# Kernel optimization log

Hardware: AMD Instinct MI355X
Metric: run time of the kernel (lower is better)

The kernel has to match this reference:

```python
import jax, jax.numpy as jnp
import numpy as np

B, N_SMI, N_ATOM, N_PROT, D = 8, 100, 45, 1000, 64


def setup_inputs() -> dict:
    key = jax.random.key(0)
    ks = jax.random.split(key, 8)
    return {
        "smi_tf": jax.random.normal(ks[0], (B, N_SMI, D), dtype=jnp.float32),
        "pro_tf": jax.random.normal(ks[1], (B, N_PROT, D), dtype=jnp.float32),
        "drug_gat": jax.random.normal(ks[2], (B, N_ATOM, D), dtype=jnp.float32),
        "w_att": jax.random.normal(ks[3], (D, D), dtype=jnp.float32) * 0.05,
        "b_att": jnp.zeros((D,), dtype=jnp.float32),
        "w1": jax.random.normal(ks[4], (2 * D, 1024), dtype=jnp.float32) * 0.05,
        "b1": jnp.zeros((1024,), dtype=jnp.float32),
        "w2": jax.random.normal(ks[5], (1024, 1024), dtype=jnp.float32) * 0.05,
        "b2": jnp.zeros((1024,), dtype=jnp.float32),
        "w3": jax.random.normal(ks[6], (1024, 512), dtype=jnp.float32) * 0.05,
        "b3": jnp.zeros((512,), dtype=jnp.float32),
        "w4": jax.random.normal(ks[7], (512, 2), dtype=jnp.float32) * 0.05,
        "b4": jnp.zeros((2,), dtype=jnp.float32),
    }


def reference(smi_tf, pro_tf, drug_gat, w_att, b_att, w1, b1, w2, b2, w3, b3, w4, b4):
    # shared attention projection on both streams
    smi_att = smi_tf @ w_att + b_att            # (B, N_smi, D)
    pro_att = pro_tf @ w_att + b_att            # (B, N_prot, D)
    smi_attss = jnp.concatenate([smi_att, drug_gat], axis=1)  # (B, Nd, D)

    # pairwise broadcast add + relu + shared linear (the big intermediate)
    pair = jax.nn.relu(smi_attss[:, :, None, :] + pro_att[:, None, :, :])  # (B, Nd, Np, D)
    atten = pair @ w_att + b_att                                           # (B, Nd, Np, D)

    # dual mean-pool gates
    smi_atts = jax.nn.sigmoid(atten.mean(axis=2))   # (B, Nd, D)
    pro_atts = jax.nn.sigmoid(atten.mean(axis=1))   # (B, Np, D)

    smi_tfs = 0.5 * smi_attss + smi_attss * smi_atts
    pro_tfs = 0.5 * pro_tf + pro_tf * pro_atts

    smi = smi_tfs.mean(axis=1)   # (B, D)
    pro = pro_tfs.mean(axis=1)   # (B, D)
    x = jnp.concatenate([smi, pro], axis=-1)  # (B, 2D)

    x = jax.nn.relu(x @ w1 + b1)
    x = jax.nn.relu(x @ w2 + b2)
    x = jax.nn.relu(x @ w3 + b3)
    return x @ w4 + b4  # (B, 2)
```

## Files before the change

kernel.cpp:

```cpp
#include <hip/hip_runtime.h>
#include <math.h>

#define B 8
#define NSMI 100
#define NATOM 45
#define ND 145
#define NP 1000
#define D 64
#define NROW 1145

#define PROJ_RPB 16
#define PROJ_BPB 72
#define ROW_BPB 37
#define COL_BPB 250
#define PAIR_ROW_BLKS (B * ROW_BPB)
#define PAIR_BLKS (PAIR_ROW_BLKS + B * COL_BPB)

__device__ __forceinline__ float4 f4z() { float4 z; z.x = z.y = z.z = z.w = 0.f; return z; }
__device__ __forceinline__ void f4acc(float4& a, const float4& v) {
    a.x += v.x; a.y += v.y; a.z += v.z; a.w += v.w;
}
__device__ __forceinline__ void acc_relu(float4& acc, const float4& a, const float4& p) {
    acc.x += fmaxf(0.f, a.x + p.x);
    acc.y += fmaxf(0.f, a.y + p.y);
    acc.z += fmaxf(0.f, a.z + p.z);
    acc.w += fmaxf(0.f, a.w + p.w);
}
__device__ __forceinline__ void wave_red_g(float4& v) {
    v.x += __shfl_xor(v.x, 16, 64); v.x += __shfl_xor(v.x, 32, 64);
    v.y += __shfl_xor(v.y, 16, 64); v.y += __shfl_xor(v.y, 32, 64);
    v.z += __shfl_xor(v.z, 16, 64); v.z += __shfl_xor(v.z, 32, 64);
    v.w += __shfl_xor(v.w, 16, 64); v.w += __shfl_xor(v.w, 32, 64);
}

__global__ __launch_bounds__(256) void k_proj2(
    const float* __restrict__ smi_tf, const float* __restrict__ pro_tf,
    const float* __restrict__ drug_gat, const float* __restrict__ w_att,
    const float* __restrict__ b_att,
    float* __restrict__ smi_attss, float* __restrict__ pro_att)
{
    int blk = blockIdx.x, t = threadIdx.x;
    int b = blk / PROJ_BPB;
    int r0 = (blk - b * PROJ_BPB) * PROJ_RPB;

    __shared__ float4 wl[64 * 17];
    __shared__ float4 rl4[16 * 17];

    #pragma unroll
    for (int i2 = 0; i2 < 4; ++i2) {
        int f = t + 256 * i2;
        float4 v = ((const float4*)w_att)[f];
        wl[(f >> 4) * 17 + (f & 15)] = v;
    }
    int rl = t >> 4, p = t & 15;
    int r = r0 + rl;
    {
        float4 v = f4z();
        if (r < NROW) {
            const float* src;
            if (r < NSMI)      src = smi_tf   + (size_t)(b * NSMI + r) * D;
            else if (r < ND)   src = drug_gat + (size_t)(b * NATOM + (r - NSMI)) * D;
            else               src = pro_tf   + (size_t)(b * NP + (r - ND)) * D;
            v = ((const float4*)src)[p];
        }
        rl4[rl * 17 + p] = v;
    }
    __syncthreads();
    if (r >= NROW) return;
    float4 out;
    if (r >= NSMI && r < ND) {
        out = rl4[rl * 17 + p];
    } else {
        float4 acc = ((const float4*)b_att)[p];
        const float* rowf = (const float*)rl4;
        #pragma unroll
        for (int k = 0; k < 64; ++k) {
            float val = rowf[rl * 68 + k];
            float4 w = wl[k * 17 + p];
            acc.x = fmaf(val, w.x, acc.x);
            acc.y = fmaf(val, w.y, acc.y);
            acc.z = fmaf(val, w.z, acc.z);
            acc.w = fmaf(val, w.w, acc.w);
        }
        out = acc;
    }
    if (r < ND) ((float4*)smi_attss)[(size_t)(b * ND + r) * 16 + p] = out;
    else        ((float4*)pro_att)[(size_t)(b * NP + (r - ND)) * 16 + p] = out;
}

__global__ __launch_bounds__(512) void k_pair(
    const float4* __restrict__ smi4, const float4* __restrict__ pro4,
    const float* __restrict__ smi_attss, const float* __restrict__ pro_tf,
    const float* __restrict__ w_att, const float* __restrict__ b_att,
    float* __restrict__ smi_tfs, float* __restrict__ pro_tfs)
{
    __shared__ float4 red[8][4][16];
    __shared__ float vl[4][64];
    int blk = blockIdx.x, t = threadIdx.x;
    int w = t >> 6, lane = t & 63, l = lane & 15, g = lane >> 4;
    int u = w * 4 + g;
    float4 acc0 = f4z(), acc1 = f4z(), acc2 = f4z(), acc3 = f4z();
    int b, base;
    bool isRow = (blk < PAIR_ROW_BLKS);

    if (isRow) {
        b = blk / ROW_BPB;
        base = (blk - b * ROW_BPB) * 4;
        float4 a0 = (base + 0 < ND) ? smi4[(size_t)(b * ND + base + 0) * 16 + l] : f4z();
        float4 a1 = (base + 1 < ND) ? smi4[(size_t)(b * ND + base + 1) * 16 + l] : f4z();
        float4 a2 = (base + 2 < ND) ? smi4[(size_t)(b * ND + base + 2) * 16 + l] : f4z();
        float4 a3 = (base + 3 < ND) ? smi4[(size_t)(b * ND + base + 3) * 16 + l] : f4z();
        const float4* pp = pro4 + (size_t)b * NP * 16 + u * 16 + l;
        #pragma unroll 4
        for (int it = 0; it < 31; ++it) {
            float4 pv = pp[it * 512];
            acc_relu(acc0, a0, pv); acc_relu(acc1, a1, pv);
            acc_relu(acc2, a2, pv); acc_relu(acc3, a3, pv);
        }
        if (u < 8) {
            float4 pv = pp[31 * 512];
            acc_relu(acc0, a0, pv); acc_relu(acc1, a1, pv);
            acc_relu(acc2, a2, pv); acc_relu(acc3, a3, pv);
        }
    } else {
        int cb = blk - PAIR_ROW_BLKS;
        b = cb / COL_BPB;
        base = (cb - b * COL_BPB) * 4;
        float4 p0 = pro4[(size_t)(b * NP + base + 0) * 16 + l];
        float4 p1 = pro4[(size_t)(b * NP + base + 1) * 16 + l];
        float4 p2 = pro4[(size_t)(b * NP + base + 2) * 16 + l];
        float4 p3 = pro4[(size_t)(b * NP + base + 3) * 16 + l];
        const float4* ap = smi4 + (size_t)b * ND * 16 + u * 16 + l;
        #pragma unroll
        for (int it = 0; it < 4; ++it) {
            float4 av = ap[it * 512];
            acc_relu(acc0, av, p0); acc_relu(acc1, av, p1);
            acc_relu(acc2, av, p2); acc_relu(acc3, av, p3);
        }
        if (u < 17) {
            float4 av = ap[4 * 512];
            acc_relu(acc0, av, p0); acc_relu(acc1, av, p1);
            acc_relu(acc2, av, p2); acc_relu(acc3, av, p3);
        }
    }

    wave_red_g(acc0); wave_red_g(acc1); wave_red_g(acc2); wave_red_g(acc3);
    if (lane < 16) {
        red[w][0][l] = acc0; red[w][1][l] = acc1;
        red[w][2][l] = acc2; red[w][3][l] = acc3;
    }
    __syncthreads();
    float invn = isRow ? (1.0f / NP) : (1.0f / ND);
    if (t < 64) {
        int ii = t >> 4, l2 = t & 15;
        float4 s = f4z();
        #pragma unroll
        for (int w2 = 0; w2 < 8; ++w2) f4acc(s, red[w2][ii][l2]);
        vl[ii][l2 * 4 + 0] = s.x * invn;
        vl[ii][l2 * 4 + 1] = s.y * invn;
        vl[ii][l2 * 4 + 2] = s.z * invn;
        vl[ii][l2 * 4 + 3] = s.w * invn;
    }
    __syncthreads();
    if (t < 256) {
        int ii = t >> 6, d = t & 63;
        int r = base + ii;
        bool ok = isRow ? (r < ND) : true;
        if (ok) {
            float m = b_att[d];
            #pragma unroll
            for (int k = 0; k < 64; ++k) m = fmaf(vl[ii][k], w_att[k * 64 + d], m);
            float gs = 1.f / (1.f + expf(-m));
            if (isRow) {
                size_t idx = (size_t)(b * ND + r) * 64 + d;
                smi_tfs[idx] = smi_attss[idx] * (0.5f + gs);
            } else {
                size_t idx = (size_t)(b * NP + r) * 64 + d;
                pro_tfs[idx] = pro_tf[idx] * (0.5f + gs);
            }
        }
    }
}

__global__ __launch_bounds__(512) void k_pool(
    const float4* __restrict__ smi_tfs4, const float4* __restrict__ pro_tfs4,
    float* __restrict__ x)
{
    __shared__ float4 ldsb[1024];
    int blk = blockIdx.x, t = threadIdx.x;
    int b = blk >> 4, s = blk & 15;
    float4 sa = f4z(), pa = f4z();
    if (t < ND) f4acc(sa, smi_tfs4[(size_t)(b * ND + t) * 16 + s]);
    for (int j = t; j < NP; j += 512) f4acc(pa, pro_tfs4[(size_t)(b * NP + j) * 16 + s]);
    ldsb[t] = sa; ldsb[512 + t] = pa;
    __syncthreads();
    for (int st = 256; st > 0; st >>= 1) {
        if (t < st) { f4acc(ldsb[t], ldsb[t + st]); f4acc(ldsb[512 + t], ldsb[512 + t + st]); }
        __syncthreads();
    }
    if (t == 0) {
        float4 S = ldsb[0], P = ldsb[512];
        x[b * 128 + s * 4 + 0] = S.x * (1.0f / ND);
        x[b * 128 + s * 4 + 1] = S.y * (1.0f / ND);
        x[b * 128 + s * 4 + 2] = S.z * (1.0f / ND);
        x[b * 128 + s * 4 + 3] = S.w * (1.0f / ND);
        x[b * 128 + 64 + s * 4 + 0] = P.x * (1.0f / NP);
        x[b * 128 + 64 + s * 4 + 1] = P.y * (1.0f / NP);
        x[b * 128 + 64 + s * 4 + 2] = P.z * (1.0f / NP);
        x[b * 128 + 64 + s * 4 + 3] = P.w * (1.0f / NP);
    }
}

__global__ __launch_bounds__(256) void k_l1(
    const float4* __restrict__ x4, const float4* __restrict__ w1_4,
    const float4* __restrict__ b1_4, float4* __restrict__ h1_4)
{
    __shared__ float lds_x[1024];
    __shared__ float4 red[2048];
    int oc = blockIdx.x, t = threadIdx.x;
    ((float4*)lds_x)[t] = x4[t];
    __syncthreads();
    int ol = t & 15, g = t >> 4;
    int o4 = oc * 16 + ol;
    float4 acc[8];
    #pragma unroll
    for (int b = 0; b < 8; ++b) acc[b] = f4z();
    #pragma unroll
    for (int kk = 0; kk < 8; ++kk) {
        int k = g * 8 + kk;
        float4 wv = w1_4[(size_t)k * 256 + o4];
        #pragma unroll
        for (int b = 0; b < 8; ++b) {
            float xv = lds_x[b * 128 + k];
            acc[b].x = fmaf(xv, wv.x, acc[b].x);
            acc[b].y = fmaf(xv, wv.y, acc[b].y);
            acc[b].z = fmaf(xv, wv.z, acc[b].z);
            acc[b].w = fmaf(xv, wv.w, acc[b].w);
        }
    }
    #pragma unroll
    for (int b = 0; b < 8; ++b) red[g * 128 + ol * 8 + b] = acc[b];
    __syncthreads();
    int u = t & 127, gg = t >> 7;
    float4 s = f4z();
    #pragma unroll
    for (int j = 0; j < 8; ++j) f4acc(s, red[(gg * 8 + j) * 128 + u]);
    red[gg * 8 * 128 + u] = s;
    __syncthreads();
    if (t < 128) {
        float4 v = red[t];
        f4acc(v, red[1024 + t]);
        int olr = t >> 3, b = t & 7;
        float4 bb = b1_4[oc * 16 + olr];
        v.x = fmaxf(v.x + bb.x, 0.f); v.y = fmaxf(v.y + bb.y, 0.f);
        v.z = fmaxf(v.z + bb.z, 0.f); v.w = fmaxf(v.w + bb.w, 0.f);
        h1_4[b * 256 + oc * 16 + olr] = v;
    }
}

__global__ __launch_bounds__(512) void k_l2(
    const float4* __restrict__ h1_4, const float4* __restrict__ w2_4,
    const float4* __restrict__ b2_4, float4* __restrict__ h2_4)
{
    __shared__ float4 buf[4096];
    float* lds_h = (float*)buf;
    int oc = blockIdx.x, t = threadIdx.x;
    #pragma unroll
    for (int j = 0; j < 4; ++j) buf[t + 512 * j] = h1_4[t + 512 * j];
    __syncthreads();
    int ol = t & 3, g = t >> 2;
    int o4 = oc * 4 + ol;
    float4 acc[8];
    #pragma unroll
    for (int b = 0; b < 8; ++b) acc[b] = f4z();
    #pragma unroll
    for (int kk = 0; kk < 8; ++kk) {
        int k = g * 8 + kk;
        float4 wv = w2_4[(size_t)k * 256 + o4];
        #pragma unroll
        for (int b = 0; b < 8; ++b) {
            float hv = lds_h[b * 1024 + k];
            acc[b].x = fmaf(hv, wv.x, acc[b].x);
            acc[b].y = fmaf(hv, wv.y, acc[b].y);
            acc[b].z = fmaf(hv, wv.z, acc[b].z);
            acc[b].w = fmaf(hv, wv.w, acc[b].w);
        }
    }
    __syncthreads();
    #pragma unroll
    for (int b = 0; b < 8; ++b) buf[g * 32 + ol * 8 + b] = acc[b];
    __syncthreads();
    int u = t & 31, gg = t >> 5;
    float4 s = f4z();
    #pragma unroll
    for (int j = 0; j < 8; ++j) f4acc(s, buf[(gg * 8 + j) * 32 + u]);
    buf[gg * 256 + u] = s;
    __syncthreads();
    if (t < 32) {
        float4 v = f4z();
        #pragma unroll
        for (int gg2 = 0; gg2 < 16; ++gg2) f4acc(v, buf[gg2 * 256 + t]);
        int olr = t >> 3, b = t & 7;
        float4 bb = b2_4[oc * 4 + olr];
        v.x = fmaxf(v.x + bb.x, 0.f); v.y = fmaxf(v.y + bb.y, 0.f);
        v.z = fmaxf(v.z + bb.z, 0.f); v.w = fmaxf(v.w + bb.w, 0.f);
        h2_4[b * 256 + oc * 4 + olr] = v;
    }
}

__global__ __launch_bounds__(512) void k_l3(
    const float4* __restrict__ h2_4, const float4* __restrict__ w3_4,
    const float4* __restrict__ b3_4, float4* __restrict__ h3_4)
{
    __shared__ float4 buf[4096];
    float* lds_h = (float*)buf;
    int oc = blockIdx.x, t = threadIdx.x;
    #pragma unroll
    for (int j = 0; j < 4; ++j) buf[t + 512 * j] = h2_4[t + 512 * j];
    __syncthreads();
    int ol = t & 3, g = t >> 2;
    int o4 = oc * 4 + ol;
    float4 acc[8];
    #pragma unroll
    for (int b = 0; b < 8; ++b) acc[b] = f4z();
    #pragma unroll
    for (int kk = 0; kk < 8; ++kk) {
        int k = g * 8 + kk;
        float4 wv = w3_4[(size_t)k * 128 + o4];
        #pragma unroll
        for (int b = 0; b < 8; ++b) {
            float hv = lds_h[b * 1024 + k];
            acc[b].x = fmaf(hv, wv.x, acc[b].x);
            acc[b].y = fmaf(hv, wv.y, acc[b].y);
            acc[b].z = fmaf(hv, wv.z, acc[b].z);
            acc[b].w = fmaf(hv, wv.w, acc[b].w);
        }
    }
    __syncthreads();
    #pragma unroll
    for (int b = 0; b < 8; ++b) buf[g * 32 + ol * 8 + b] = acc[b];
    __syncthreads();
    int u = t & 31, gg = t >> 5;
    float4 s = f4z();
    #pragma unroll
    for (int j = 0; j < 8; ++j) f4acc(s, buf[(gg * 8 + j) * 32 + u]);
    buf[gg * 256 + u] = s;
    __syncthreads();
    if (t < 32) {
        float4 v = f4z();
        #pragma unroll
        for (int gg2 = 0; gg2 < 16; ++gg2) f4acc(v, buf[gg2 * 256 + t]);
        int olr = t >> 3, b = t & 7;
        float4 bb = b3_4[oc * 4 + olr];
        v.x = fmaxf(v.x + bb.x, 0.f); v.y = fmaxf(v.y + bb.y, 0.f);
        v.z = fmaxf(v.z + bb.z, 0.f); v.w = fmaxf(v.w + bb.w, 0.f);
        h3_4[b * 128 + oc * 4 + olr] = v;
    }
}

__global__ __launch_bounds__(512) void k_l4(
    const float* __restrict__ h3, const float* __restrict__ w4p,
    const float* __restrict__ b4p, float* __restrict__ out)
{
    __shared__ float h3s[4096];
    __shared__ float w4s[1024];
    __shared__ float red[8][8][2];
    int t = threadIdx.x;
    ((float4*)h3s)[t] = ((const float4*)h3)[t];
    ((float4*)h3s)[t + 512] = ((const float4*)h3)[t + 512];
    if (t < 256) ((float4*)w4s)[t] = ((const float4*)w4p)[t];
    __syncthreads();
    int w = t >> 6, lane = t & 63;
    #pragma unroll
    for (int b = 0; b < 8; ++b) {
        float hv = h3s[b * 512 + t];
        float v0 = hv * w4s[t * 2];
        float v1 = hv * w4s[t * 2 + 1];
        #pragma unroll
        for (int off = 32; off > 0; off >>= 1) {
            v0 += __shfl_xor(v0, off, 64);
            v1 += __shfl_xor(v1, off, 64);
        }
        if (lane == 0) { red[w][b][0] = v0; red[w][b][1] = v1; }
    }
    __syncthreads();
    if (t < 16) {
        int b = t >> 1, o = t & 1;
        float s = b4p[o];
        #pragma unroll
        for (int w2 = 0; w2 < 8; ++w2) s += red[w2][b][o];
        out[b * 2 + o] = s;
    }
}

extern "C" void kernel_launch(void* const* d_in, const int* in_sizes, int n_in,
                              void* d_out, int out_size, void* d_ws, size_t ws_size,
                              hipStream_t stream)
{
    const float* smi_tf   = (const float*)d_in[0];
    const float* pro_tf   = (const float*)d_in[1];
    const float* drug_gat = (const float*)d_in[2];
    const float* w_att    = (const float*)d_in[3];
    const float* b_att    = (const float*)d_in[4];
    const float* w1 = (const float*)d_in[5];
    const float* b1 = (const float*)d_in[6];
    const float* w2 = (const float*)d_in[7];
    const float* b2 = (const float*)d_in[8];
    const float* w3 = (const float*)d_in[9];
    const float* b3 = (const float*)d_in[10];
    const float* w4 = (const float*)d_in[11];
    const float* b4 = (const float*)d_in[12];
    float* out = (float*)d_out;

    float* ws = (float*)d_ws;
    float* smi_attss = ws;
    float* pro_att   = smi_attss + 74240;
    float* smi_tfs   = pro_att + 512000;
    float* pro_tfs   = smi_tfs + 74240;
    float* x   = pro_tfs + 512000;
    float* h1  = x + 1024;
    float* h2  = h1 + 8192;
    float* h3  = h2 + 8192;

    k_proj2<<<B * PROJ_BPB, 256, 0, stream>>>(smi_tf, pro_tf, drug_gat, w_att, b_att,
                                              smi_attss, pro_att);
    k_pair <<<PAIR_BLKS, 512, 0, stream>>>((const float4*)smi_attss, (const float4*)pro_att,
                                           smi_attss, pro_tf, w_att, b_att, smi_tfs, pro_tfs);
    k_pool <<<128, 512, 0, stream>>>((const float4*)smi_tfs, (const float4*)pro_tfs, x);
    k_l1   <<<16, 256, 0, stream>>>((const float4*)x, (const float4*)w1,
                                    (const float4*)b1, (float4*)h1);
    k_l2   <<<64, 512, 0, stream>>>((const float4*)h1, (const float4*)w2,
                                    (const float4*)b2, (float4*)h2);
    k_l3   <<<32, 512, 0, stream>>>((const float4*)h2, (const float4*)w3,
                                    (const float4*)b3, (float4*)h3);
    k_l4   <<<1, 512, 0, stream>>>(h3, w4, b4, out);
}
```

Before: 129.8 us.

## Fuse pooling into pair kernel via atomics and merge MLP layers

The gated outputs are no longer written to global memory and re-read by a separate pooling kernel. The pair kernel now reduces its four rows in shared memory and atomically adds column sums into a small buffer, which the projection kernel zeroes. Layer 1 is recomputed redundantly in every block of the fused layer 1+2 kernel, and layers 3 and 4 are fused with atomic accumulation into the output. Seven launches become four, at the cost of atomic contention and redundant layer-1 work, and the float sums are no longer deterministic.

```diff
diff --git a/kernel.cpp b/kernel.cpp
--- a/kernel.cpp
+++ b/kernel.cpp
@@ -37,9 +37,14 @@
     const float* __restrict__ smi_tf, const float* __restrict__ pro_tf,
     const float* __restrict__ drug_gat, const float* __restrict__ w_att,
     const float* __restrict__ b_att,
-    float* __restrict__ smi_attss, float* __restrict__ pro_att)
+    float* __restrict__ smi_attss, float* __restrict__ pro_att,
+    float* __restrict__ x_sums, float* __restrict__ out)
 {
     int blk = blockIdx.x, t = threadIdx.x;
+    if (blk == 0) {
+        ((float4*)x_sums)[t] = f4z();
+        if (t < 16) out[t] = 0.f;
+    }
     int b = blk / PROJ_BPB;
     int r0 = (blk - b * PROJ_BPB) * PROJ_RPB;
 
@@ -67,9 +72,9 @@
     }
     __syncthreads();
     if (r >= NROW) return;
-    float4 out;
+    float4 out4;
     if (r >= NSMI && r < ND) {
-        out = rl4[rl * 17 + p];
+        out4 = rl4[rl * 17 + p];
     } else {
         float4 acc = ((const float4*)b_att)[p];
         const float* rowf = (const float*)rl4;
@@ -82,20 +87,21 @@
             acc.z = fmaf(val, w.z, acc.z);
             acc.w = fmaf(val, w.w, acc.w);
         }
-        out = acc;
-    }
-    if (r < ND) ((float4*)smi_attss)[(size_t)(b * ND + r) * 16 + p] = out;
-    else        ((float4*)pro_att)[(size_t)(b * NP + (r - ND)) * 16 + p] = out;
+        out4 = acc;
+    }
+    if (r < ND) ((float4*)smi_attss)[(size_t)(b * ND + r) * 16 + p] = out4;
+    else        ((float4*)pro_att)[(size_t)(b * NP + (r - ND)) * 16 + p] = out4;
 }
 
 __global__ __launch_bounds__(512) void k_pair(
     const float4* __restrict__ smi4, const float4* __restrict__ pro4,
     const float* __restrict__ smi_attss, const float* __restrict__ pro_tf,
     const float* __restrict__ w_att, const float* __restrict__ b_att,
-    float* __restrict__ smi_tfs, float* __restrict__ pro_tfs)
+    float* __restrict__ x_sums)
 {
     __shared__ float4 red[8][4][16];
     __shared__ float vl[4][64];
+    __shared__ float gv[4][64];
     int blk = blockIdx.x, t = threadIdx.x;
     int w = t >> 6, lane = t & 63, l = lane & 15, g = lane >> 4;
     int u = w * 4 + g;
@@ -166,107 +172,122 @@
         int ii = t >> 6, d = t & 63;
         int r = base + ii;
         bool ok = isRow ? (r < ND) : true;
+        float v = 0.f;
         if (ok) {
             float m = b_att[d];
             #pragma unroll
             for (int k = 0; k < 64; ++k) m = fmaf(vl[ii][k], w_att[k * 64 + d], m);
             float gs = 1.f / (1.f + expf(-m));
-            if (isRow) {
-                size_t idx = (size_t)(b * ND + r) * 64 + d;
-                smi_tfs[idx] = smi_attss[idx] * (0.5f + gs);
-            } else {
-                size_t idx = (size_t)(b * NP + r) * 64 + d;
-                pro_tfs[idx] = pro_tf[idx] * (0.5f + gs);
-            }
-        }
-    }
-}
-
-__global__ __launch_bounds__(512) void k_pool(
-    const float4* __restrict__ smi_tfs4, const float4* __restrict__ pro_tfs4,
-    float* __restrict__ x)
-{
-    __shared__ float4 ldsb[1024];
-    int blk = blockIdx.x, t = threadIdx.x;
-    int b = blk >> 4, s = blk & 15;
-    float4 sa = f4z(), pa = f4z();
-    if (t < ND) f4acc(sa, smi_tfs4[(size_t)(b * ND + t) * 16 + s]);
-    for (int j = t; j < NP; j += 512) f4acc(pa, pro_tfs4[(size_t)(b * NP + j) * 16 + s]);
-    ldsb[t] = sa; ldsb[512 + t] = pa;
-    __syncthreads();
-    for (int st = 256; st > 0; st >>= 1) {
-        if (t < st) { f4acc(ldsb[t], ldsb[t + st]); f4acc(ldsb[512 + t], ldsb[512 + t + st]); }
-        __syncthreads();
-    }
-    if (t == 0) {
-        float4 S = ldsb[0], P = ldsb[512];
-        x[b * 128 + s * 4 + 0] = S.x * (1.0f / ND);
-        x[b * 128 + s * 4 + 1] = S.y * (1.0f / ND);
-        x[b * 128 + s * 4 + 2] = S.z * (1.0f / ND);
-        x[b * 128 + s * 4 + 3] = S.w * (1.0f / ND);
-        x[b * 128 + 64 + s * 4 + 0] = P.x * (1.0f / NP);
-        x[b * 128 + 64 + s * 4 + 1] = P.y * (1.0f / NP);
-        x[b * 128 + 64 + s * 4 + 2] = P.z * (1.0f / NP);
-        x[b * 128 + 64 + s * 4 + 3] = P.w * (1.0f / NP);
-    }
-}
-
-__global__ __launch_bounds__(256) void k_l1(
-    const float4* __restrict__ x4, const float4* __restrict__ w1_4,
-    const float4* __restrict__ b1_4, float4* __restrict__ h1_4)
-{
-    __shared__ float lds_x[1024];
-    __shared__ float4 red[2048];
+            size_t idx = isRow ? ((size_t)(b * ND + r) * 64 + d)
+                               : ((size_t)(b * NP + r) * 64 + d);
+            v = (isRow ? smi_attss[idx] : pro_tf[idx]) * (0.5f + gs);
+        }
+        gv[ii][d] = v;
+    }
+    __syncthreads();
+    if (t < 64) {
+        float s = gv[0][t] + gv[1][t] + gv[2][t] + gv[3][t];
+        atomicAdd(&x_sums[b * 128 + (isRow ? 0 : 64) + t], s);
+    }
+}
+
+__global__ __launch_bounds__(512) void k_l12(
+    const float* __restrict__ x_sums, const float4* __restrict__ w1_4,
+    const float* __restrict__ b1, const float4* __restrict__ w2_4,
+    const float* __restrict__ b2, float4* __restrict__ h2_4)
+{
+    __shared__ float4 buf[4096];
+    float* xs  = (float*)buf;
+    float* h1f = (float*)buf + 1024;
+    float4* h1f4 = buf + 256;
     int oc = blockIdx.x, t = threadIdx.x;
-    ((float4*)lds_x)[t] = x4[t];
-    __syncthreads();
-    int ol = t & 15, g = t >> 4;
-    int o4 = oc * 16 + ol;
+    xs[t]       = x_sums[t]       * (((t & 127) < 64) ? (1.0f / ND) : (1.0f / NP));
+    xs[t + 512] = x_sums[t + 512] * (((t & 127) < 64) ? (1.0f / ND) : (1.0f / NP));
+    __syncthreads();
+    {
+        int o4 = t & 255, bh = t >> 8;
+        const float* x0 = xs + (bh * 4 + 0) * 128;
+        const float* x1 = xs + (bh * 4 + 1) * 128;
+        const float* x2 = xs + (bh * 4 + 2) * 128;
+        const float* x3 = xs + (bh * 4 + 3) * 128;
+        float4 a0 = f4z(), a1 = f4z(), a2 = f4z(), a3 = f4z();
+        #pragma unroll 8
+        for (int k = 0; k < 128; ++k) {
+            float4 wv = w1_4[(size_t)k * 256 + o4];
+            a0.x = fmaf(x0[k], wv.x, a0.x); a0.y = fmaf(x0[k], wv.y, a0.y);
+            a0.z = fmaf(x0[k], wv.z, a0.z); a0.w = fmaf(x0[k], wv.w, a0.w);
+            a1.x = fmaf(x1[k], wv.x, a1.x); a1.y = fmaf(x1[k], wv.y, a1.y);
+            a1.z = fmaf(x1[k], wv.z, a1.z); a1.w = fmaf(x1[k], wv.w, a1.w);
+            a2.x = fmaf(x2[k], wv.x, a2.x); a2.y = fmaf(x2[k], wv.y, a2.y);
+            a2.z = fmaf(x2[k], wv.z, a2.z); a2.w = fmaf(x2[k], wv.w, a2.w);
+            a3.x = fmaf(x3[k], wv.x, a3.x); a3.y = fmaf(x3[k], wv.y, a3.y);
+            a3.z = fmaf(x3[k], wv.z, a3.z); a3.w = fmaf(x3[k], wv.w, a3.w);
+        }
+        float4 bb = ((const float4*)b1)[o4];
+        a0.x = fmaxf(a0.x + bb.x, 0.f); a0.y = fmaxf(a0.y + bb.y, 0.f);
+        a0.z = fmaxf(a0.z + bb.z, 0.f); a0.w = fmaxf(a0.w + bb.w, 0.f);
+        a1.x = fmaxf(a1.x + bb.x, 0.f); a1.y = fmaxf(a1.y + bb.y, 0.f);
+        a1.z = fmaxf(a1.z + bb.z, 0.f); a1.w = fmaxf(a1.w + bb.w, 0.f);
+        a2.x = fmaxf(a2.x + bb.x, 0.f); a2.y = fmaxf(a2.y + bb.y, 0.f);
+        a2.z = fmaxf(a2.z + bb.z, 0.f); a2.w = fmaxf(a2.w + bb.w, 0.f);
+        a3.x = fmaxf(a3.x + bb.x, 0.f); a3.y = fmaxf(a3.y + bb.y, 0.f);
+        a3.z = fmaxf(a3.z + bb.z, 0.f); a3.w = fmaxf(a3.w + bb.w, 0.f);
+        h1f4[(size_t)(bh * 4 + 0) * 256 + o4] = a0;
+        h1f4[(size_t)(bh * 4 + 1) * 256 + o4] = a1;
+        h1f4[(size_t)(bh * 4 + 2) * 256 + o4] = a2;
+        h1f4[(size_t)(bh * 4 + 3) * 256 + o4] = a3;
+    }
+    __syncthreads();
+    int ol = t & 3, g = t >> 2;
+    int o4g = oc * 4 + ol;
     float4 acc[8];
     #pragma unroll
     for (int b = 0; b < 8; ++b) acc[b] = f4z();
     #pragma unroll
     for (int kk = 0; kk < 8; ++kk) {
         int k = g * 8 + kk;
-        float4 wv = w1_4[(size_t)k * 256 + o4];
+        float4 wv = w2_4[(size_t)k * 256 + o4g];
         #pragma unroll
         for (int b = 0; b < 8; ++b) {
-            float xv = lds_x[b * 128 + k];
-            acc[b].x = fmaf(xv, wv.x, acc[b].x);
-            acc[b].y = fmaf(xv, wv.y, acc[b].y);
-            acc[b].z = fmaf(xv, wv.z, acc[b].z);
-            acc[b].w = fmaf(xv, wv.w, acc[b].w);
-        }
-    }
-    #pragma unroll
-    for (int b = 0; b < 8; ++b) red[g * 128 + ol * 8 + b] = acc[b];
-    __syncthreads();
-    int u = t & 127, gg = t >> 7;
+            float hv = h1f[b * 1024 + k];
+            acc[b].x = fmaf(hv, wv.x, acc[b].x);
+            acc[b].y = fmaf(hv, wv.y, acc[b].y);
+            acc[b].z = fmaf(hv, wv.z, acc[b].z);
+            acc[b].w = fmaf(hv, wv.w, acc[b].w);
+        }
+    }
+    __syncthreads();
+    #pragma unroll
+    for (int b = 0; b < 8; ++b) buf[g * 32 + ol * 8 + b] = acc[b];
+    __syncthreads();
+    int u = t & 31, gg = t >> 5;
     float4 s = f4z();
     #pragma unroll
-    for (int j = 0; j < 8; ++j) f4acc(s, red[(gg * 8 + j) * 128 + u]);
-    red[gg * 8 * 128 + u] = s;
-    __syncthreads();
-    if (t < 128) {
-        float4 v = red[t];
-        f4acc(v, red[1024 + t]);
+    for (int j = 0; j < 8; ++j) f4acc(s, buf[(gg * 8 + j) * 32 + u]);
+    buf[gg * 256 + u] = s;
+    __syncthreads();
+    if (t < 32) {
+        float4 v = f4z();
+        #pragma unroll
+        for (int gg2 = 0; gg2 < 16; ++gg2) f4acc(v, buf[gg2 * 256 + t]);
         int olr = t >> 3, b = t & 7;
-        float4 bb = b1_4[oc * 16 + olr];
+        float4 bb = ((const float4*)b2)[oc * 4 + olr];
         v.x = fmaxf(v.x + bb.x, 0.f); v.y = fmaxf(v.y + bb.y, 0.f);
         v.z = fmaxf(v.z + bb.z, 0.f); v.w = fmaxf(v.w + bb.w, 0.f);
-        h1_4[b * 256 + oc * 16 + olr] = v;
-    }
-}
-
-__global__ __launch_bounds__(512) void k_l2(
-    const float4* __restrict__ h1_4, const float4* __restrict__ w2_4,
-    const float4* __restrict__ b2_4, float4* __restrict__ h2_4)
+        h2_4[b * 256 + oc * 4 + olr] = v;
+    }
+}
+
+__global__ __launch_bounds__(512) void k_l34(
+    const float4* __restrict__ h2_4, const float4* __restrict__ w3_4,
+    const float* __restrict__ b3, const float* __restrict__ w4p,
+    const float* __restrict__ b4p, float* __restrict__ out)
 {
     __shared__ float4 buf[4096];
     float* lds_h = (float*)buf;
     int oc = blockIdx.x, t = threadIdx.x;
     #pragma unroll
-    for (int j = 0; j < 4; ++j) buf[t + 512 * j] = h1_4[t + 512 * j];
+    for (int j = 0; j < 4; ++j) buf[t + 512 * j] = h2_4[t + 512 * j];
     __syncthreads();
     int ol = t & 3, g = t >> 2;
     int o4 = oc * 4 + ol;
@@ -276,7 +297,7 @@
     #pragma unroll
     for (int kk = 0; kk < 8; ++kk) {
         int k = g * 8 + kk;
-        float4 wv = w2_4[(size_t)k * 256 + o4];
+        float4 wv = w3_4[(size_t)k * 128 + o4];
         #pragma unroll
         for (int b = 0; b < 8; ++b) {
             float hv = lds_h[b * 1024 + k];
@@ -301,95 +322,21 @@
         #pragma unroll
         for (int gg2 = 0; gg2 < 16; ++gg2) f4acc(v, buf[gg2 * 256 + t]);
         int olr = t >> 3, b = t & 7;
-        float4 bb = b2_4[oc * 4 + olr];
+        float4 bb = ((const float4*)b3)[oc * 4 + olr];
         v.x = fmaxf(v.x + bb.x, 0.f); v.y = fmaxf(v.y + bb.y, 0.f);
         v.z = fmaxf(v.z + bb.z, 0.f); v.w = fmaxf(v.w + bb.w, 0.f);
-        h2_4[b * 256 + oc * 4 + olr] = v;
-    }
-}
-
-__global__ __launch_bounds__(512) void k_l3(
-    const float4* __restrict__ h2_4, const float4* __restrict__ w3_4,
-    const float4* __restrict__ b3_4, float4* __restrict__ h3_4)
-{
-    __shared__ float4 buf[4096];
-    float* lds_h = (float*)buf;
-    int oc = blockIdx.x, t = threadIdx.x;
-    #pragma unroll
-    for (int j = 0; j < 4; ++j) buf[t + 512 * j] = h2_4[t + 512 * j];
-    __syncthreads();
-    int ol = t & 3, g = t >> 2;
-    int o4 = oc * 4 + ol;
-    float4 acc[8];
-    #pragma unroll
-    for (int b = 0; b < 8; ++b) acc[b] = f4z();
-    #pragma unroll
-    for (int kk = 0; kk < 8; ++kk) {
-        int k = g * 8 + kk;
-        float4 wv = w3_4[(size_t)k * 128 + o4];
-        #pragma unroll
-        for (int b = 0; b < 8; ++b) {
-            float hv = lds_h[b * 1024 + k];
-            acc[b].x = fmaf(hv, wv.x, acc[b].x);
-            acc[b].y = fmaf(hv, wv.y, acc[b].y);
-            acc[b].z = fmaf(hv, wv.z, acc[b].z);
-            acc[b].w = fmaf(hv, wv.w, acc[b].w);
-        }
-    }
-    __syncthreads();
-    #pragma unroll
-    for (int b = 0; b < 8; ++b) buf[g * 32 + ol * 8 + b] = acc[b];
-    __syncthreads();
-    int u = t & 31, gg = t >> 5;
-    float4 s = f4z();
-    #pragma unroll
-    for (int j = 0; j < 8; ++j) f4acc(s, buf[(gg * 8 + j) * 32 + u]);
-    buf[gg * 256 + u] = s;
-    __syncthreads();
-    if (t < 32) {
-        float4 v = f4z();
-        #pragma unroll
-        for (int gg2 = 0; gg2 < 16; ++gg2) f4acc(v, buf[gg2 * 256 + t]);
-        int olr = t >> 3, b = t & 7;
-        float4 bb = b3_4[oc * 4 + olr];
-        v.x = fmaxf(v.x + bb.x, 0.f); v.y = fmaxf(v.y + bb.y, 0.f);
-        v.z = fmaxf(v.z + bb.z, 0.f); v.w = fmaxf(v.w + bb.w, 0.f);
-        h3_4[b * 128 + oc * 4 + olr] = v;
-    }
-}
-
-__global__ __launch_bounds__(512) void k_l4(
-    const float* __restrict__ h3, const float* __restrict__ w4p,
-    const float* __restrict__ b4p, float* __restrict__ out)
-{
-    __shared__ float h3s[4096];
-    __shared__ float w4s[1024];
-    __shared__ float red[8][8][2];
-    int t = threadIdx.x;
-    ((float4*)h3s)[t] = ((const float4*)h3)[t];
-    ((float4*)h3s)[t + 512] = ((const float4*)h3)[t + 512];
-    if (t < 256) ((float4*)w4s)[t] = ((const float4*)w4p)[t];
-    __syncthreads();
-    int w = t >> 6, lane = t & 63;
-    #pragma unroll
-    for (int b = 0; b < 8; ++b) {
-        float hv = h3s[b * 512 + t];
-        float v0 = hv * w4s[t * 2];
-        float v1 = hv * w4s[t * 2 + 1];
-        #pragma unroll
-        for (int off = 32; off > 0; off >>= 1) {
-            v0 += __shfl_xor(v0, off, 64);
-            v1 += __shfl_xor(v1, off, 64);
-        }
-        if (lane == 0) { red[w][b][0] = v0; red[w][b][1] = v1; }
-    }
-    __syncthreads();
-    if (t < 16) {
-        int b = t >> 1, o = t & 1;
-        float s = b4p[o];
-        #pragma unroll
-        for (int w2 = 0; w2 < 8; ++w2) s += red[w2][b][o];
-        out[b * 2 + o] = s;
+        int ob = oc * 16 + olr * 4;
+        float p0 = v.x * w4p[(ob + 0) * 2] + v.y * w4p[(ob + 1) * 2]
+                 + v.z * w4p[(ob + 2) * 2] + v.w * w4p[(ob + 3) * 2];
+        float p1 = v.x * w4p[(ob + 0) * 2 + 1] + v.y * w4p[(ob + 1) * 2 + 1]
+                 + v.z * w4p[(ob + 2) * 2 + 1] + v.w * w4p[(ob + 3) * 2 + 1];
+        p0 += __shfl_xor(p0, 8, 64);  p0 += __shfl_xor(p0, 16, 64);
+        p1 += __shfl_xor(p1, 8, 64);  p1 += __shfl_xor(p1, 16, 64);
+        if (olr == 0) {
+            if (oc == 0) { p0 += b4p[0]; p1 += b4p[1]; }
+            atomicAdd(&out[b * 2 + 0], p0);
+            atomicAdd(&out[b * 2 + 1], p1);
+        }
     }
 }
 
@@ -415,23 +362,15 @@
     float* ws = (float*)d_ws;
     float* smi_attss = ws;
     float* pro_att   = smi_attss + 74240;
-    float* smi_tfs   = pro_att + 512000;
-    float* pro_tfs   = smi_tfs + 74240;
-    float* x   = pro_tfs + 512000;
-    float* h1  = x + 1024;
-    float* h2  = h1 + 8192;
-    float* h3  = h2 + 8192;
+    float* x_sums    = pro_att + 512000;
+    float* h2        = x_sums + 1024;
 
     k_proj2<<<B * PROJ_BPB, 256, 0, stream>>>(smi_tf, pro_tf, drug_gat, w_att, b_att,
-                                              smi_attss, pro_att);
+                                              smi_attss, pro_att, x_sums, out);
     k_pair <<<PAIR_BLKS, 512, 0, stream>>>((const float4*)smi_attss, (const float4*)pro_att,
-                                           smi_attss, pro_tf, w_att, b_att, smi_tfs, pro_tfs);
-    k_pool <<<128, 512, 0, stream>>>((const float4*)smi_tfs, (const float4*)pro_tfs, x);
-    k_l1   <<<16, 256, 0, stream>>>((const float4*)x, (const float4*)w1,
-                                    (const float4*)b1, (float4*)h1);
-    k_l2   <<<64, 512, 0, stream>>>((const float4*)h1, (const float4*)w2,
-                                    (const float4*)b2, (float4*)h2);
-    k_l3   <<<32, 512, 0, stream>>>((const float4*)h2, (const float4*)w3,
-                                    (const float4*)b3, (float4*)h3);
-    k_l4   <<<1, 512, 0, stream>>>(h3, w4, b4, out);
-}
+                                           smi_attss, pro_tf, w_att, b_att, x_sums);
+    k_l12  <<<64, 512, 0, stream>>>(x_sums, (const float4*)w1, b1,
+                                    (const float4*)w2, b2, (float4*)h2);
+    k_l34  <<<32, 512, 0, stream>>>((const float4*)h2, (const float4*)w3, b3,
+                                    w4, b4, out);
+}
```

Result: slower. 133.8 us (+3.1%).
